# Optimization experiments

Hardware: AMD Instinct MI355X
Metric: run time of the kernel (lower is better)

Reference implementation:

```python
import jax, jax.numpy as jnp
import numpy as np

EPS = 1e-6

def rmsnorm(x, w):
    rms = jnp.sqrt(jnp.mean(x * x, axis=-1, keepdims=True) + EPS)
    return w * x / rms

def setup_inputs() -> dict:
    key = jax.random.key(0)
    k1, k2, k3 = jax.random.split(key, 3)
    S, N, B, T, D = 8, 8, 2, 2048, 1024
    return {
        "pseudo_queries": jax.random.normal(k1, (S, D), dtype=jnp.float32),
        "block_reps": jax.random.normal(k2, (N, B, T, D), dtype=jnp.float32),
        "partial_sums": jax.random.normal(k3, (S, B, T, D), dtype=jnp.float32),
        "norm_weight": jnp.ones((D,), dtype=jnp.float32),
    }

def reference(pseudo_queries, block_reps, partial_sums, norm_weight):
    D = pseudo_queries.shape[-1]
    scale = 1.0 / jnp.sqrt(jnp.asarray(D, pseudo_queries.dtype))

    # ---- Phase 1: inter-block attention over the N layers ----
    V = block_reps                               # [N,B,T,D]
    K = rmsnorm(V, norm_weight)                  # [N,B,T,D]
    logits = jnp.einsum('sd,nbtd->snbt', pseudo_queries, K) * scale  # [S,N,B,T]
    inter_max = jnp.max(logits, axis=1)          # [S,B,T]
    exp_logits = jnp.exp(logits - inter_max[:, None])
    inter_lse = jnp.log(jnp.sum(exp_logits, axis=1)) + inter_max     # [S,B,T]
    attn = jax.nn.softmax(logits, axis=1)        # [S,N,B,T]
    inter_out = jnp.einsum('snbt,nbtd->sbtd', attn, V)               # [S,B,T,D]

    # ---- Phase 2: intra-block merge (vectorized over S) ----
    K2 = rmsnorm(partial_sums, norm_weight)      # [S,B,T,D]
    intra_max = jnp.einsum('sd,sbtd->sbt', pseudo_queries, K2) * scale  # [S,B,T]
    merged_max = jnp.maximum(inter_max, intra_max)
    w_inter = jnp.exp(inter_max - merged_max)
    w_intra = jnp.exp(intra_max - merged_max)
    merged_lse = jnp.log(w_inter * jnp.exp(inter_lse - inter_max) + w_intra) + merged_max
    norm = w_inter + w_intra
    merged_out = (w_inter[..., None] * inter_out + w_intra[..., None] * partial_sums) / norm[..., None]
    return merged_out, merged_max, merged_lse
```

## Files before the change

### kernel.cpp

```cpp
#include <hip/hip_runtime.h>
#include <math.h>

#define TPB 256

template <int CTRL>
__device__ __forceinline__ float dpp_add(float x) {
    int yi = __builtin_amdgcn_update_dpp(0, __float_as_int(x), CTRL, 0xF, 0xF, true);
    return x + __int_as_float(yi);
}

__device__ __forceinline__ float wave_sum(float x) {
    x = dpp_add<0xB1>(x);
    x = dpp_add<0x4E>(x);
    x = dpp_add<0x141>(x);
    x = dpp_add<0x140>(x);
    x = dpp_add<0x142>(x);
    x = dpp_add<0x143>(x);
    return __int_as_float(__builtin_amdgcn_readlane(__float_as_int(x), 63));
}

__device__ __forceinline__ float dot4(const float4& a, const float4& b) {
    return a.x * b.x + a.y * b.y + a.z * b.z + a.w * b.w;
}

__global__ __launch_bounds__(TPB) void two_phase_attn_kernel(
    const float* __restrict__ q,
    const float* __restrict__ V,
    const float* __restrict__ P,
    const float* __restrict__ wgt,
    float* __restrict__ out)
{
    constexpr int    N   = 8;
    constexpr int    D   = 1024;
    constexpr int    BT  = 4096;
    constexpr size_t ROW = (size_t)BT * D;
    constexpr size_t OUT_MM  = (size_t)8 * ROW;
    constexpr size_t OUT_LSE = OUT_MM + (size_t)BT * 8;
    constexpr float  SCALE = 0.03125f;
    constexpr float  EPS   = 1e-6f;

    __shared__ float sV[N][D];

    const int bt   = blockIdx.x;
    const int tid  = threadIdx.x;
    const int w    = tid >> 6;
    const int lane = tid & 63;
    const int s0 = 2 * w, s1 = s0 + 1;
    const size_t btD = (size_t)bt * D;

    #pragma unroll
    for (int j = 0; j < 4; ++j) {
        const int d = j * 256 + lane * 4;
        *(float4*)(&sV[s0][d]) = *(const float4*)(V + (size_t)s0 * ROW + btD + d);
        *(float4*)(&sV[s1][d]) = *(const float4*)(V + (size_t)s1 * ROW + btD + d);
    }
    __syncthreads();

    float dot0[N], dot1[N], vsq[N];
    #pragma unroll
    for (int n = 0; n < N; ++n) { dot0[n] = 0.f; dot1[n] = 0.f; vsq[n] = 0.f; }

    #pragma unroll
    for (int j = 0; j < 4; ++j) {
        const int d = j * 256 + lane * 4;
        const float4 wv = *(const float4*)(wgt + d);
        const float4 a  = *(const float4*)(q + s0 * D + d);
        const float4 b  = *(const float4*)(q + s1 * D + d);
        const float4 qa = make_float4(a.x*wv.x, a.y*wv.y, a.z*wv.z, a.w*wv.w);
        const float4 qb = make_float4(b.x*wv.x, b.y*wv.y, b.z*wv.z, b.w*wv.w);
        #pragma unroll
        for (int n = 0; n < N; ++n) {
            const float4 v = *(const float4*)(&sV[n][d]);
            dot0[n] += dot4(qa, v);
            dot1[n] += dot4(qb, v);
            vsq[n]  += dot4(v, v);
        }
    }

    float4 p0[4], p1[4];
    #pragma unroll
    for (int j = 0; j < 4; ++j) {
        const int d = j * 256 + lane * 4;
        p0[j] = *(const float4*)(P + (size_t)s0 * ROW + btD + d);
        p1[j] = *(const float4*)(P + (size_t)s1 * ROW + btD + d);
    }

    #pragma unroll
    for (int n = 0; n < N; ++n) {
        dot0[n] = wave_sum(dot0[n]);
        dot1[n] = wave_sum(dot1[n]);
        vsq[n]  = wave_sum(vsq[n]);
    }

    float e0[N], e1[N];
    float m0 = -1e30f, m1 = -1e30f;
    #pragma unroll
    for (int n = 0; n < N; ++n) {
        const float rinv = rsqrtf(vsq[n] * (1.0f / 1024.0f) + EPS);
        e0[n] = dot0[n] * rinv * SCALE;  m0 = fmaxf(m0, e0[n]);
        e1[n] = dot1[n] * rinv * SCALE;  m1 = fmaxf(m1, e1[n]);
    }
    float es0 = 0.f, es1 = 0.f;
    #pragma unroll
    for (int n = 0; n < N; ++n) {
        e0[n] = __expf(e0[n] - m0);  es0 += e0[n];
        e1[n] = __expf(e1[n] - m1);  es1 += e1[n];
    }

    float ssq20 = 0.f, ssq21 = 0.f, dp0 = 0.f, dp1 = 0.f;
    #pragma unroll
    for (int j = 0; j < 4; ++j) {
        const int d = j * 256 + lane * 4;
        const float4 wv = *(const float4*)(wgt + d);
        const float4 a  = *(const float4*)(q + s0 * D + d);
        const float4 b  = *(const float4*)(q + s1 * D + d);
        ssq20 += dot4(p0[j], p0[j]);
        ssq21 += dot4(p1[j], p1[j]);
        dp0 += (a.x*wv.x)*p0[j].x + (a.y*wv.y)*p0[j].y + (a.z*wv.z)*p0[j].z + (a.w*wv.w)*p0[j].w;
        dp1 += (b.x*wv.x)*p1[j].x + (b.y*wv.y)*p1[j].y + (b.z*wv.z)*p1[j].z + (b.w*wv.w)*p1[j].w;
    }
    ssq20 = wave_sum(ssq20);  ssq21 = wave_sum(ssq21);
    dp0   = wave_sum(dp0);    dp1   = wave_sum(dp1);

    const float im0 = dp0 * rsqrtf(ssq20 * (1.0f/1024.0f) + EPS) * SCALE;
    const float im1 = dp1 * rsqrtf(ssq21 * (1.0f/1024.0f) + EPS) * SCALE;

    const float mm0 = fmaxf(m0, im0),    mm1 = fmaxf(m1, im1);
    const float wi0 = __expf(m0 - mm0),  wi1 = __expf(m1 - mm1);
    const float wa0 = __expf(im0 - mm0), wa1 = __expf(im1 - mm1);
    const float lse0 = __logf(wi0 * es0 + wa0) + mm0;
    const float lse1 = __logf(wi1 * es1 + wa1) + mm1;
    const float nrm0 = wi0 + wa0,        nrm1 = wi1 + wa1;
    const float cA0 = wi0 / (es0 * nrm0), cA1 = wi1 / (es1 * nrm1);
    const float cp0 = wa0 / nrm0,         cp1 = wa1 / nrm1;

    #pragma unroll
    for (int j = 0; j < 4; ++j) {
        const int d = j * 256 + lane * 4;
        float4 A0 = make_float4(0.f, 0.f, 0.f, 0.f);
        float4 A1 = make_float4(0.f, 0.f, 0.f, 0.f);
        #pragma unroll
        for (int n = 0; n < N; ++n) {
            const float4 v = *(const float4*)(&sV[n][d]);
            A0.x += e0[n]*v.x; A0.y += e0[n]*v.y; A0.z += e0[n]*v.z; A0.w += e0[n]*v.w;
            A1.x += e1[n]*v.x; A1.y += e1[n]*v.y; A1.z += e1[n]*v.z; A1.w += e1[n]*v.w;
        }
        float4 o0, o1;
        o0.x = cA0*A0.x + cp0*p0[j].x;  o0.y = cA0*A0.y + cp0*p0[j].y;
        o0.z = cA0*A0.z + cp0*p0[j].z;  o0.w = cA0*A0.w + cp0*p0[j].w;
        o1.x = cA1*A1.x + cp1*p1[j].x;  o1.y = cA1*A1.y + cp1*p1[j].y;
        o1.z = cA1*A1.z + cp1*p1[j].z;  o1.w = cA1*A1.w + cp1*p1[j].w;
        *(float4*)(out + (size_t)s0 * ROW + btD + d) = o0;
        *(float4*)(out + (size_t)s1 * ROW + btD + d) = o1;
    }
    if (lane == 0) {
        out[OUT_MM  + (size_t)s0 * BT + bt] = mm0;
        out[OUT_MM  + (size_t)s1 * BT + bt] = mm1;
        out[OUT_LSE + (size_t)s0 * BT + bt] = lse0;
        out[OUT_LSE + (size_t)s1 * BT + bt] = lse1;
    }
}

extern "C" void kernel_launch(void* const* d_in, const int* in_sizes, int n_in,
                              void* d_out, int out_size, void* d_ws, size_t ws_size,
                              hipStream_t stream) {
    const float* q   = (const float*)d_in[0];
    const float* V   = (const float*)d_in[1];
    const float* P   = (const float*)d_in[2];
    const float* wgt = (const float*)d_in[3];
    float* o = (float*)d_out;

    two_phase_attn_kernel<<<4096, TPB, 0, stream>>>(q, V, P, wgt, o);
}
```

Baseline: 105.1 us.

## Make blocks persistent over eight rows with register-prefetched V double buffering

Each block now processes eight consecutive bt rows instead of one, launching 512 blocks instead of 4096. The V row for the next iteration is prefetched into registers while the current row is computed, then written to shared memory after a barrier. This aims to hide global load latency and amortise launch and setup costs. The trade-offs are fewer resident blocks (512 blocks over the GPU's compute units), higher register pressure and an extra barrier per iteration.

```diff
diff --git a/kernel.cpp b/kernel.cpp
--- a/kernel.cpp
+++ b/kernel.cpp
@@ -1,7 +1,9 @@
 #include <hip/hip_runtime.h>
 #include <math.h>
 
-#define TPB 256
+#define TPB   256
+#define NBLK  512
+#define ITERS 8
 
 template <int CTRL>
 __device__ __forceinline__ float dpp_add(float x) {
@@ -19,8 +21,8 @@
     return __int_as_float(__builtin_amdgcn_readlane(__float_as_int(x), 63));
 }
 
-__device__ __forceinline__ float dot4(const float4& a, const float4& b) {
-    return a.x * b.x + a.y * b.y + a.z * b.z + a.w * b.w;
+__device__ __forceinline__ float dot4(const float4 a, const float4 b) {
+    return a.x*b.x + a.y*b.y + a.z*b.z + a.w*b.w;
 }
 
 __global__ __launch_bounds__(TPB) void two_phase_attn_kernel(
@@ -41,123 +43,158 @@
 
     __shared__ float sV[N][D];
 
-    const int bt   = blockIdx.x;
     const int tid  = threadIdx.x;
     const int w    = tid >> 6;
     const int lane = tid & 63;
-    const int s0 = 2 * w, s1 = s0 + 1;
-    const size_t btD = (size_t)bt * D;
-
+    const int s0 = 2*w, s1 = s0 + 1;
+    const int d0 = lane * 4;
+    const int bt0 = blockIdx.x * ITERS;
+
+    const float* Vr0 = V + (size_t)s0*ROW + (size_t)bt0*D + d0;
+    const float* Vr1 = V + (size_t)s1*ROW + (size_t)bt0*D + d0;
+    const float* Pr0 = P + (size_t)s0*ROW + (size_t)bt0*D + d0;
+    const float* Pr1 = P + (size_t)s1*ROW + (size_t)bt0*D + d0;
+    float*       Or0 = out + (size_t)s0*ROW + (size_t)bt0*D + d0;
+    float*       Or1 = out + (size_t)s1*ROW + (size_t)bt0*D + d0;
+
+    float4 vst0[4], vst1[4];
     #pragma unroll
     for (int j = 0; j < 4; ++j) {
-        const int d = j * 256 + lane * 4;
-        *(float4*)(&sV[s0][d]) = *(const float4*)(V + (size_t)s0 * ROW + btD + d);
-        *(float4*)(&sV[s1][d]) = *(const float4*)(V + (size_t)s1 * ROW + btD + d);
-    }
-    __syncthreads();
-
-    float dot0[N], dot1[N], vsq[N];
-    #pragma unroll
-    for (int n = 0; n < N; ++n) { dot0[n] = 0.f; dot1[n] = 0.f; vsq[n] = 0.f; }
-
+        vst0[j] = *(const float4*)(Vr0 + j*256);
+        vst1[j] = *(const float4*)(Vr1 + j*256);
+    }
     #pragma unroll
     for (int j = 0; j < 4; ++j) {
-        const int d = j * 256 + lane * 4;
-        const float4 wv = *(const float4*)(wgt + d);
-        const float4 a  = *(const float4*)(q + s0 * D + d);
-        const float4 b  = *(const float4*)(q + s1 * D + d);
-        const float4 qa = make_float4(a.x*wv.x, a.y*wv.y, a.z*wv.z, a.w*wv.w);
-        const float4 qb = make_float4(b.x*wv.x, b.y*wv.y, b.z*wv.z, b.w*wv.w);
-        #pragma unroll
-        for (int n = 0; n < N; ++n) {
-            const float4 v = *(const float4*)(&sV[n][d]);
-            dot0[n] += dot4(qa, v);
-            dot1[n] += dot4(qb, v);
-            vsq[n]  += dot4(v, v);
-        }
-    }
-
-    float4 p0[4], p1[4];
+        *(float4*)(&sV[s0][j*256 + d0]) = vst0[j];
+        *(float4*)(&sV[s1][j*256 + d0]) = vst1[j];
+    }
     #pragma unroll
     for (int j = 0; j < 4; ++j) {
-        const int d = j * 256 + lane * 4;
-        p0[j] = *(const float4*)(P + (size_t)s0 * ROW + btD + d);
-        p1[j] = *(const float4*)(P + (size_t)s1 * ROW + btD + d);
-    }
-
-    #pragma unroll
-    for (int n = 0; n < N; ++n) {
-        dot0[n] = wave_sum(dot0[n]);
-        dot1[n] = wave_sum(dot1[n]);
-        vsq[n]  = wave_sum(vsq[n]);
-    }
-
-    float e0[N], e1[N];
-    float m0 = -1e30f, m1 = -1e30f;
-    #pragma unroll
-    for (int n = 0; n < N; ++n) {
-        const float rinv = rsqrtf(vsq[n] * (1.0f / 1024.0f) + EPS);
-        e0[n] = dot0[n] * rinv * SCALE;  m0 = fmaxf(m0, e0[n]);
-        e1[n] = dot1[n] * rinv * SCALE;  m1 = fmaxf(m1, e1[n]);
-    }
-    float es0 = 0.f, es1 = 0.f;
-    #pragma unroll
-    for (int n = 0; n < N; ++n) {
-        e0[n] = __expf(e0[n] - m0);  es0 += e0[n];
-        e1[n] = __expf(e1[n] - m1);  es1 += e1[n];
-    }
-
-    float ssq20 = 0.f, ssq21 = 0.f, dp0 = 0.f, dp1 = 0.f;
-    #pragma unroll
-    for (int j = 0; j < 4; ++j) {
-        const int d = j * 256 + lane * 4;
-        const float4 wv = *(const float4*)(wgt + d);
-        const float4 a  = *(const float4*)(q + s0 * D + d);
-        const float4 b  = *(const float4*)(q + s1 * D + d);
-        ssq20 += dot4(p0[j], p0[j]);
-        ssq21 += dot4(p1[j], p1[j]);
-        dp0 += (a.x*wv.x)*p0[j].x + (a.y*wv.y)*p0[j].y + (a.z*wv.z)*p0[j].z + (a.w*wv.w)*p0[j].w;
-        dp1 += (b.x*wv.x)*p1[j].x + (b.y*wv.y)*p1[j].y + (b.z*wv.z)*p1[j].z + (b.w*wv.w)*p1[j].w;
-    }
-    ssq20 = wave_sum(ssq20);  ssq21 = wave_sum(ssq21);
-    dp0   = wave_sum(dp0);    dp1   = wave_sum(dp1);
-
-    const float im0 = dp0 * rsqrtf(ssq20 * (1.0f/1024.0f) + EPS) * SCALE;
-    const float im1 = dp1 * rsqrtf(ssq21 * (1.0f/1024.0f) + EPS) * SCALE;
-
-    const float mm0 = fmaxf(m0, im0),    mm1 = fmaxf(m1, im1);
-    const float wi0 = __expf(m0 - mm0),  wi1 = __expf(m1 - mm1);
-    const float wa0 = __expf(im0 - mm0), wa1 = __expf(im1 - mm1);
-    const float lse0 = __logf(wi0 * es0 + wa0) + mm0;
-    const float lse1 = __logf(wi1 * es1 + wa1) + mm1;
-    const float nrm0 = wi0 + wa0,        nrm1 = wi1 + wa1;
-    const float cA0 = wi0 / (es0 * nrm0), cA1 = wi1 / (es1 * nrm1);
-    const float cp0 = wa0 / nrm0,         cp1 = wa1 / nrm1;
-
-    #pragma unroll
-    for (int j = 0; j < 4; ++j) {
-        const int d = j * 256 + lane * 4;
-        float4 A0 = make_float4(0.f, 0.f, 0.f, 0.f);
-        float4 A1 = make_float4(0.f, 0.f, 0.f, 0.f);
+        vst0[j] = *(const float4*)(Vr0 + D + j*256);
+        vst1[j] = *(const float4*)(Vr1 + D + j*256);
+    }
+    __syncthreads();
+
+    for (int k = 0; k < ITERS; ++k) {
+        const int off = k * D;
+
+        float4 p0[4], p1[4];
+        #pragma unroll
+        for (int j = 0; j < 4; ++j) {
+            p0[j] = *(const float4*)(Pr0 + off + j*256);
+            p1[j] = *(const float4*)(Pr1 + off + j*256);
+        }
+
+        float dot0[N], dot1[N], vsq[N];
+        #pragma unroll
+        for (int n = 0; n < N; ++n) { dot0[n] = 0.f; dot1[n] = 0.f; vsq[n] = 0.f; }
+        #pragma unroll
+        for (int j = 0; j < 4; ++j) {
+            const int d = j*256 + d0;
+            const float4 wv = *(const float4*)(wgt + d);
+            const float4 a  = *(const float4*)(q + s0*D + d);
+            const float4 b  = *(const float4*)(q + s1*D + d);
+            const float4 qa = make_float4(a.x*wv.x, a.y*wv.y, a.z*wv.z, a.w*wv.w);
+            const float4 qb = make_float4(b.x*wv.x, b.y*wv.y, b.z*wv.z, b.w*wv.w);
+            #pragma unroll
+            for (int n = 0; n < N; ++n) {
+                const float4 v = *(const float4*)(&sV[n][d]);
+                dot0[n] += dot4(qa, v);
+                dot1[n] += dot4(qb, v);
+                vsq[n]  += dot4(v, v);
+            }
+        }
         #pragma unroll
         for (int n = 0; n < N; ++n) {
-            const float4 v = *(const float4*)(&sV[n][d]);
-            A0.x += e0[n]*v.x; A0.y += e0[n]*v.y; A0.z += e0[n]*v.z; A0.w += e0[n]*v.w;
-            A1.x += e1[n]*v.x; A1.y += e1[n]*v.y; A1.z += e1[n]*v.z; A1.w += e1[n]*v.w;
-        }
-        float4 o0, o1;
-        o0.x = cA0*A0.x + cp0*p0[j].x;  o0.y = cA0*A0.y + cp0*p0[j].y;
-        o0.z = cA0*A0.z + cp0*p0[j].z;  o0.w = cA0*A0.w + cp0*p0[j].w;
-        o1.x = cA1*A1.x + cp1*p1[j].x;  o1.y = cA1*A1.y + cp1*p1[j].y;
-        o1.z = cA1*A1.z + cp1*p1[j].z;  o1.w = cA1*A1.w + cp1*p1[j].w;
-        *(float4*)(out + (size_t)s0 * ROW + btD + d) = o0;
-        *(float4*)(out + (size_t)s1 * ROW + btD + d) = o1;
-    }
-    if (lane == 0) {
-        out[OUT_MM  + (size_t)s0 * BT + bt] = mm0;
-        out[OUT_MM  + (size_t)s1 * BT + bt] = mm1;
-        out[OUT_LSE + (size_t)s0 * BT + bt] = lse0;
-        out[OUT_LSE + (size_t)s1 * BT + bt] = lse1;
+            dot0[n] = wave_sum(dot0[n]);
+            dot1[n] = wave_sum(dot1[n]);
+            vsq[n]  = wave_sum(vsq[n]);
+        }
+
+        float e0[N], e1[N];
+        float m0 = -1e30f, m1 = -1e30f;
+        #pragma unroll
+        for (int n = 0; n < N; ++n) {
+            const float rinv = rsqrtf(vsq[n] * (1.0f/1024.0f) + EPS);
+            e0[n] = dot0[n] * rinv * SCALE;  m0 = fmaxf(m0, e0[n]);
+            e1[n] = dot1[n] * rinv * SCALE;  m1 = fmaxf(m1, e1[n]);
+        }
+        float es0 = 0.f, es1 = 0.f;
+        #pragma unroll
+        for (int n = 0; n < N; ++n) {
+            e0[n] = __expf(e0[n] - m0);  es0 += e0[n];
+            e1[n] = __expf(e1[n] - m1);  es1 += e1[n];
+        }
+
+        float ssq20 = 0.f, ssq21 = 0.f, dp0 = 0.f, dp1 = 0.f;
+        #pragma unroll
+        for (int j = 0; j < 4; ++j) {
+            const int d = j*256 + d0;
+            const float4 wv = *(const float4*)(wgt + d);
+            const float4 a  = *(const float4*)(q + s0*D + d);
+            const float4 b  = *(const float4*)(q + s1*D + d);
+            ssq20 += dot4(p0[j], p0[j]);
+            ssq21 += dot4(p1[j], p1[j]);
+            dp0 += (a.x*wv.x)*p0[j].x + (a.y*wv.y)*p0[j].y + (a.z*wv.z)*p0[j].z + (a.w*wv.w)*p0[j].w;
+            dp1 += (b.x*wv.x)*p1[j].x + (b.y*wv.y)*p1[j].y + (b.z*wv.z)*p1[j].z + (b.w*wv.w)*p1[j].w;
+        }
+        ssq20 = wave_sum(ssq20);  ssq21 = wave_sum(ssq21);
+        dp0   = wave_sum(dp0);    dp1   = wave_sum(dp1);
+
+        const float im0 = dp0 * rsqrtf(ssq20 * (1.0f/1024.0f) + EPS) * SCALE;
+        const float im1 = dp1 * rsqrtf(ssq21 * (1.0f/1024.0f) + EPS) * SCALE;
+        const float mm0 = fmaxf(m0, im0),    mm1 = fmaxf(m1, im1);
+        const float wi0 = __expf(m0 - mm0),  wi1 = __expf(m1 - mm1);
+        const float wa0 = __expf(im0 - mm0), wa1 = __expf(im1 - mm1);
+        const float lse0 = __logf(wi0 * es0 + wa0) + mm0;
+        const float lse1 = __logf(wi1 * es1 + wa1) + mm1;
+        const float nrm0 = wi0 + wa0,        nrm1 = wi1 + wa1;
+        const float cA0 = wi0 / (es0 * nrm0), cA1 = wi1 / (es1 * nrm1);
+        const float cp0 = wa0 / nrm0,         cp1 = wa1 / nrm1;
+
+        #pragma unroll
+        for (int j = 0; j < 4; ++j) {
+            const int d = j*256 + d0;
+            float4 A0 = make_float4(0.f,0.f,0.f,0.f);
+            float4 A1 = make_float4(0.f,0.f,0.f,0.f);
+            #pragma unroll
+            for (int n = 0; n < N; ++n) {
+                const float4 v = *(const float4*)(&sV[n][d]);
+                A0.x += e0[n]*v.x; A0.y += e0[n]*v.y; A0.z += e0[n]*v.z; A0.w += e0[n]*v.w;
+                A1.x += e1[n]*v.x; A1.y += e1[n]*v.y; A1.z += e1[n]*v.z; A1.w += e1[n]*v.w;
+            }
+            float4 o0, o1;
+            o0.x = cA0*A0.x + cp0*p0[j].x;  o0.y = cA0*A0.y + cp0*p0[j].y;
+            o0.z = cA0*A0.z + cp0*p0[j].z;  o0.w = cA0*A0.w + cp0*p0[j].w;
+            o1.x = cA1*A1.x + cp1*p1[j].x;  o1.y = cA1*A1.y + cp1*p1[j].y;
+            o1.z = cA1*A1.z + cp1*p1[j].z;  o1.w = cA1*A1.w + cp1*p1[j].w;
+            *(float4*)(Or0 + off + j*256) = o0;
+            *(float4*)(Or1 + off + j*256) = o1;
+        }
+        if (lane == 0) {
+            const int bt = bt0 + k;
+            out[OUT_MM  + (size_t)s0*BT + bt] = mm0;
+            out[OUT_MM  + (size_t)s1*BT + bt] = mm1;
+            out[OUT_LSE + (size_t)s0*BT + bt] = lse0;
+            out[OUT_LSE + (size_t)s1*BT + bt] = lse1;
+        }
+
+        __syncthreads();
+        if (k + 1 < ITERS) {
+            #pragma unroll
+            for (int j = 0; j < 4; ++j) {
+                *(float4*)(&sV[s0][j*256 + d0]) = vst0[j];
+                *(float4*)(&sV[s1][j*256 + d0]) = vst1[j];
+            }
+            if (k + 2 < ITERS) {
+                #pragma unroll
+                for (int j = 0; j < 4; ++j) {
+                    vst0[j] = *(const float4*)(Vr0 + (k+2)*D + j*256);
+                    vst1[j] = *(const float4*)(Vr1 + (k+2)*D + j*256);
+                }
+            }
+            __syncthreads();
+        }
     }
 }
 
@@ -170,5 +207,5 @@
     const float* wgt = (const float*)d_in[3];
     float* o = (float*)d_out;
 
-    two_phase_attn_kernel<<<4096, TPB, 0, stream>>>(q, V, P, wgt, o);
-}
+    two_phase_attn_kernel<<<NBLK, TPB, 0, stream>>>(q, V, P, wgt, o);
+}
```

Measured after the change: 164.9 us. +56.9%, slower.

## Use one wave per pseudo-query and compute V sum-of-squares once per row

Applied to the files above, without the earlier changes.

The block grows from 4 to 8 waves, so each wave handles a single pseudo-query instead of two. Each wave loads its own V and P rows into registers and computes the V squared norm once, sharing it through shared memory. This removes the redundant per-wave recomputation of all eight V norms and halves per-thread register state, which should allow more waves in flight to hide memory latency. The cost is more waves contending for LDS reads and a larger block per bt, and the launch_bounds hint of 8 may constrain register allocation.

```diff
diff --git a/kernel.cpp b/kernel.cpp
--- a/kernel.cpp
+++ b/kernel.cpp
@@ -1,7 +1,7 @@
 #include <hip/hip_runtime.h>
 #include <math.h>
 
-#define TPB 256
+#define TPB 512
 
 template <int CTRL>
 __device__ __forceinline__ float dpp_add(float x) {
@@ -19,11 +19,11 @@
     return __int_as_float(__builtin_amdgcn_readlane(__float_as_int(x), 63));
 }
 
-__device__ __forceinline__ float dot4(const float4& a, const float4& b) {
-    return a.x * b.x + a.y * b.y + a.z * b.z + a.w * b.w;
+__device__ __forceinline__ float dot4(const float4 a, const float4 b) {
+    return a.x*b.x + a.y*b.y + a.z*b.z + a.w*b.w;
 }
 
-__global__ __launch_bounds__(TPB) void two_phase_attn_kernel(
+__global__ __launch_bounds__(TPB, 8) void two_phase_attn_kernel(
     const float* __restrict__ q,
     const float* __restrict__ V,
     const float* __restrict__ P,
@@ -40,124 +40,103 @@
     constexpr float  EPS   = 1e-6f;
 
     __shared__ float sV[N][D];
+    __shared__ float sSsq[N];
 
-    const int bt   = blockIdx.x;
     const int tid  = threadIdx.x;
     const int w    = tid >> 6;
     const int lane = tid & 63;
-    const int s0 = 2 * w, s1 = s0 + 1;
+    const int d0   = lane * 4;
+    const int bt   = blockIdx.x;
     const size_t btD = (size_t)bt * D;
+
+    const float* Vr = V   + (size_t)w * ROW + btD + d0;
+    const float* Pr = P   + (size_t)w * ROW + btD + d0;
+    float*       Or = out + (size_t)w * ROW + btD + d0;
+
+    float4 v[4], p[4], qw[4];
+    #pragma unroll
+    for (int j = 0; j < 4; ++j) v[j] = *(const float4*)(Vr + j*256);
+    #pragma unroll
+    for (int j = 0; j < 4; ++j) p[j] = *(const float4*)(Pr + j*256);
+    #pragma unroll
+    for (int j = 0; j < 4; ++j) {
+        const int d = j*256 + d0;
+        const float4 a  = *(const float4*)(q + w*D + d);
+        const float4 wv = *(const float4*)(wgt + d);
+        qw[j] = make_float4(a.x*wv.x, a.y*wv.y, a.z*wv.z, a.w*wv.w);
+    }
+
+    float vsq = 0.f;
+    #pragma unroll
+    for (int j = 0; j < 4; ++j) {
+        *(float4*)(&sV[w][j*256 + d0]) = v[j];
+        vsq += dot4(v[j], v[j]);
+    }
+    vsq = wave_sum(vsq);
+    if (lane == 0) sSsq[w] = vsq;
+    __syncthreads();
+
+    float dt[N];
+    #pragma unroll
+    for (int n = 0; n < N; ++n) dt[n] = 0.f;
+    #pragma unroll
+    for (int j = 0; j < 4; ++j) {
+        const int d = j*256 + d0;
+        #pragma unroll
+        for (int n = 0; n < N; ++n)
+            dt[n] += dot4(qw[j], *(const float4*)(&sV[n][d]));
+    }
+    #pragma unroll
+    for (int n = 0; n < N; ++n) dt[n] = wave_sum(dt[n]);
+
+    float m = -1e30f;
+    #pragma unroll
+    for (int n = 0; n < N; ++n) {
+        const float rinv = rsqrtf(sSsq[n] * (1.0f/1024.0f) + EPS);
+        dt[n] = dt[n] * rinv * SCALE;
+        m = fmaxf(m, dt[n]);
+    }
+    float es = 0.f;
+    #pragma unroll
+    for (int n = 0; n < N; ++n) { dt[n] = __expf(dt[n] - m); es += dt[n]; }
+
+    float ssq2 = 0.f, dp = 0.f;
+    #pragma unroll
+    for (int j = 0; j < 4; ++j) {
+        ssq2 += dot4(p[j], p[j]);
+        dp   += dot4(qw[j], p[j]);
+    }
+    ssq2 = wave_sum(ssq2);
+    dp   = wave_sum(dp);
+
+    const float im  = dp * rsqrtf(ssq2 * (1.0f/1024.0f) + EPS) * SCALE;
+    const float mm  = fmaxf(m, im);
+    const float wi  = __expf(m  - mm);
+    const float wa  = __expf(im - mm);
+    const float lse = __logf(wi * es + wa) + mm;
+    const float nrm = wi + wa;
+    const float cA  = wi / (es * nrm);
+    const float cp  = wa / nrm;
 
     #pragma unroll
     for (int j = 0; j < 4; ++j) {
-        const int d = j * 256 + lane * 4;
-        *(float4*)(&sV[s0][d]) = *(const float4*)(V + (size_t)s0 * ROW + btD + d);
-        *(float4*)(&sV[s1][d]) = *(const float4*)(V + (size_t)s1 * ROW + btD + d);
-    }
-    __syncthreads();
-
-    float dot0[N], dot1[N], vsq[N];
-    #pragma unroll
-    for (int n = 0; n < N; ++n) { dot0[n] = 0.f; dot1[n] = 0.f; vsq[n] = 0.f; }
-
-    #pragma unroll
-    for (int j = 0; j < 4; ++j) {
-        const int d = j * 256 + lane * 4;
-        const float4 wv = *(const float4*)(wgt + d);
-        const float4 a  = *(const float4*)(q + s0 * D + d);
-        const float4 b  = *(const float4*)(q + s1 * D + d);
-        const float4 qa = make_float4(a.x*wv.x, a.y*wv.y, a.z*wv.z, a.w*wv.w);
-        const float4 qb = make_float4(b.x*wv.x, b.y*wv.y, b.z*wv.z, b.w*wv.w);
+        const int d = j*256 + d0;
+        float4 A = make_float4(0.f, 0.f, 0.f, 0.f);
         #pragma unroll
         for (int n = 0; n < N; ++n) {
-            const float4 v = *(const float4*)(&sV[n][d]);
-            dot0[n] += dot4(qa, v);
-            dot1[n] += dot4(qb, v);
-            vsq[n]  += dot4(v, v);
+            const float4 vv = *(const float4*)(&sV[n][d]);
+            A.x += dt[n]*vv.x; A.y += dt[n]*vv.y; A.z += dt[n]*vv.z; A.w += dt[n]*vv.w;
         }
-    }
-
-    float4 p0[4], p1[4];
-    #pragma unroll
-    for (int j = 0; j < 4; ++j) {
-        const int d = j * 256 + lane * 4;
-        p0[j] = *(const float4*)(P + (size_t)s0 * ROW + btD + d);
-        p1[j] = *(const float4*)(P + (size_t)s1 * ROW + btD + d);
-    }
-
-    #pragma unroll
-    for (int n = 0; n < N; ++n) {
-        dot0[n] = wave_sum(dot0[n]);
-        dot1[n] = wave_sum(dot1[n]);
-        vsq[n]  = wave_sum(vsq[n]);
-    }
-
-    float e0[N], e1[N];
-    float m0 = -1e30f, m1 = -1e30f;
-    #pragma unroll
-    for (int n = 0; n < N; ++n) {
-        const float rinv = rsqrtf(vsq[n] * (1.0f / 1024.0f) + EPS);
-        e0[n] = dot0[n] * rinv * SCALE;  m0 = fmaxf(m0, e0[n]);
-        e1[n] = dot1[n] * rinv * SCALE;  m1 = fmaxf(m1, e1[n]);
-    }
-    float es0 = 0.f, es1 = 0.f;
-    #pragma unroll
-    for (int n = 0; n < N; ++n) {
-        e0[n] = __expf(e0[n] - m0);  es0 += e0[n];
-        e1[n] = __expf(e1[n] - m1);  es1 += e1[n];
-    }
-
-    float ssq20 = 0.f, ssq21 = 0.f, dp0 = 0.f, dp1 = 0.f;
-    #pragma unroll
-    for (int j = 0; j < 4; ++j) {
-        const int d = j * 256 + lane * 4;
-        const float4 wv = *(const float4*)(wgt + d);
-        const float4 a  = *(const float4*)(q + s0 * D + d);
-        const float4 b  = *(const float4*)(q + s1 * D + d);
-        ssq20 += dot4(p0[j], p0[j]);
-        ssq21 += dot4(p1[j], p1[j]);
-        dp0 += (a.x*wv.x)*p0[j].x + (a.y*wv.y)*p0[j].y + (a.z*wv.z)*p0[j].z + (a.w*wv.w)*p0[j].w;
-        dp1 += (b.x*wv.x)*p1[j].x + (b.y*wv.y)*p1[j].y + (b.z*wv.z)*p1[j].z + (b.w*wv.w)*p1[j].w;
-    }
-    ssq20 = wave_sum(ssq20);  ssq21 = wave_sum(ssq21);
-    dp0   = wave_sum(dp0);    dp1   = wave_sum(dp1);
-
-    const float im0 = dp0 * rsqrtf(ssq20 * (1.0f/1024.0f) + EPS) * SCALE;
-    const float im1 = dp1 * rsqrtf(ssq21 * (1.0f/1024.0f) + EPS) * SCALE;
-
-    const float mm0 = fmaxf(m0, im0),    mm1 = fmaxf(m1, im1);
-    const float wi0 = __expf(m0 - mm0),  wi1 = __expf(m1 - mm1);
-    const float wa0 = __expf(im0 - mm0), wa1 = __expf(im1 - mm1);
-    const float lse0 = __logf(wi0 * es0 + wa0) + mm0;
-    const float lse1 = __logf(wi1 * es1 + wa1) + mm1;
-    const float nrm0 = wi0 + wa0,        nrm1 = wi1 + wa1;
-    const float cA0 = wi0 / (es0 * nrm0), cA1 = wi1 / (es1 * nrm1);
-    const float cp0 = wa0 / nrm0,         cp1 = wa1 / nrm1;
-
-    #pragma unroll
-    for (int j = 0; j < 4; ++j) {
-        const int d = j * 256 + lane * 4;
-        float4 A0 = make_float4(0.f, 0.f, 0.f, 0.f);
-        float4 A1 = make_float4(0.f, 0.f, 0.f, 0.f);
-        #pragma unroll
-        for (int n = 0; n < N; ++n) {
-            const float4 v = *(const float4*)(&sV[n][d]);
-            A0.x += e0[n]*v.x; A0.y += e0[n]*v.y; A0.z += e0[n]*v.z; A0.w += e0[n]*v.w;
-            A1.x += e1[n]*v.x; A1.y += e1[n]*v.y; A1.z += e1[n]*v.z; A1.w += e1[n]*v.w;
-        }
-        float4 o0, o1;
-        o0.x = cA0*A0.x + cp0*p0[j].x;  o0.y = cA0*A0.y + cp0*p0[j].y;
-        o0.z = cA0*A0.z + cp0*p0[j].z;  o0.w = cA0*A0.w + cp0*p0[j].w;
-        o1.x = cA1*A1.x + cp1*p1[j].x;  o1.y = cA1*A1.y + cp1*p1[j].y;
-        o1.z = cA1*A1.z + cp1*p1[j].z;  o1.w = cA1*A1.w + cp1*p1[j].w;
-        *(float4*)(out + (size_t)s0 * ROW + btD + d) = o0;
-        *(float4*)(out + (size_t)s1 * ROW + btD + d) = o1;
+        float4 o;
+        o.x = cA*A.x + cp*p[j].x;
+        o.y = cA*A.y + cp*p[j].y;
+        o.z = cA*A.z + cp*p[j].z;
+        o.w = cA*A.w + cp*p[j].w;
+        *(float4*)(Or + j*256) = o;
     }
     if (lane == 0) {
-        out[OUT_MM  + (size_t)s0 * BT + bt] = mm0;
-        out[OUT_MM  + (size_t)s1 * BT + bt] = mm1;
-        out[OUT_LSE + (size_t)s0 * BT + bt] = lse0;
-        out[OUT_LSE + (size_t)s1 * BT + bt] = lse1;
+        out[OUT_MM  + (size_t)w * BT + bt] = mm;
+        out[OUT_LSE + (size_t)w * BT + bt] = lse;
     }
 }
 
```

Measured after the change: 147.3 us. 1.4x slower.

## Split work per (bt, s-pair) block with V held in registers

Applied to the files above, without the earlier changes.

Launches four blocks per token, each handling one pair of pseudo-queries across the full hidden dimension with one float4 per thread, instead of one block per token staging all layer rows in shared memory. V rows are kept in registers and partial dot products are reduced across waves through a small shared buffer. This removes the large shared-memory footprint to raise occupancy, and adds a launch bound hint. The cost is that each token's V rows are read by four blocks, relying on cache to absorb the extra traffic, plus a block-wide reduction and barrier.

```diff
diff --git a/kernel.cpp b/kernel.cpp
--- a/kernel.cpp
+++ b/kernel.cpp
@@ -19,11 +19,11 @@
     return __int_as_float(__builtin_amdgcn_readlane(__float_as_int(x), 63));
 }
 
-__device__ __forceinline__ float dot4(const float4& a, const float4& b) {
-    return a.x * b.x + a.y * b.y + a.z * b.z + a.w * b.w;
+__device__ __forceinline__ float dot4(const float4 a, const float4 b) {
+    return a.x*b.x + a.y*b.y + a.z*b.z + a.w*b.w;
 }
 
-__global__ __launch_bounds__(TPB) void two_phase_attn_kernel(
+__global__ __launch_bounds__(TPB, 4) void two_phase_attn_kernel(
     const float* __restrict__ q,
     const float* __restrict__ V,
     const float* __restrict__ P,
@@ -31,74 +31,70 @@
     float* __restrict__ out)
 {
     constexpr int    N   = 8;
+    constexpr int    BT  = 4096;
     constexpr int    D   = 1024;
-    constexpr int    BT  = 4096;
     constexpr size_t ROW = (size_t)BT * D;
     constexpr size_t OUT_MM  = (size_t)8 * ROW;
     constexpr size_t OUT_LSE = OUT_MM + (size_t)BT * 8;
     constexpr float  SCALE = 0.03125f;
     constexpr float  EPS   = 1e-6f;
 
-    __shared__ float sV[N][D];
+    __shared__ float red[28][4];
 
-    const int bt   = blockIdx.x;
     const int tid  = threadIdx.x;
     const int w    = tid >> 6;
     const int lane = tid & 63;
-    const int s0 = 2 * w, s1 = s0 + 1;
+    const int idx  = blockIdx.x;
+    const int bt   = idx >> 2;
+    const int sp   = idx & 3;
+    const int s0   = 2*sp, s1 = 2*sp + 1;
+    const int d0   = tid * 4;
     const size_t btD = (size_t)bt * D;
 
+    float4 v[N];
     #pragma unroll
-    for (int j = 0; j < 4; ++j) {
-        const int d = j * 256 + lane * 4;
-        *(float4*)(&sV[s0][d]) = *(const float4*)(V + (size_t)s0 * ROW + btD + d);
-        *(float4*)(&sV[s1][d]) = *(const float4*)(V + (size_t)s1 * ROW + btD + d);
+    for (int n = 0; n < N; ++n)
+        v[n] = *(const float4*)(V + (size_t)n * ROW + btD + d0);
+    const float4 p0 = *(const float4*)(P + (size_t)s0 * ROW + btD + d0);
+    const float4 p1 = *(const float4*)(P + (size_t)s1 * ROW + btD + d0);
+    const float4 a0 = *(const float4*)(q + s0 * D + d0);
+    const float4 a1 = *(const float4*)(q + s1 * D + d0);
+    const float4 wv = *(const float4*)(wgt + d0);
+    const float4 qw0 = make_float4(a0.x*wv.x, a0.y*wv.y, a0.z*wv.z, a0.w*wv.w);
+    const float4 qw1 = make_float4(a1.x*wv.x, a1.y*wv.y, a1.z*wv.z, a1.w*wv.w);
+
+    float r[28];
+    #pragma unroll
+    for (int n = 0; n < N; ++n) {
+        r[n]      = dot4(qw0, v[n]);
+        r[8 + n]  = dot4(qw1, v[n]);
+        r[16 + n] = dot4(v[n], v[n]);
+    }
+    r[24] = dot4(p0, p0);
+    r[25] = dot4(p1, p1);
+    r[26] = dot4(qw0, p0);
+    r[27] = dot4(qw1, p1);
+
+    #pragma unroll
+    for (int i = 0; i < 28; ++i) r[i] = wave_sum(r[i]);
+    if (lane == 0) {
+        #pragma unroll
+        for (int i = 0; i < 28; ++i) red[i][w] = r[i];
     }
     __syncthreads();
-
-    float dot0[N], dot1[N], vsq[N];
     #pragma unroll
-    for (int n = 0; n < N; ++n) { dot0[n] = 0.f; dot1[n] = 0.f; vsq[n] = 0.f; }
-
-    #pragma unroll
-    for (int j = 0; j < 4; ++j) {
-        const int d = j * 256 + lane * 4;
-        const float4 wv = *(const float4*)(wgt + d);
-        const float4 a  = *(const float4*)(q + s0 * D + d);
-        const float4 b  = *(const float4*)(q + s1 * D + d);
-        const float4 qa = make_float4(a.x*wv.x, a.y*wv.y, a.z*wv.z, a.w*wv.w);
-        const float4 qb = make_float4(b.x*wv.x, b.y*wv.y, b.z*wv.z, b.w*wv.w);
-        #pragma unroll
-        for (int n = 0; n < N; ++n) {
-            const float4 v = *(const float4*)(&sV[n][d]);
-            dot0[n] += dot4(qa, v);
-            dot1[n] += dot4(qb, v);
-            vsq[n]  += dot4(v, v);
-        }
-    }
-
-    float4 p0[4], p1[4];
-    #pragma unroll
-    for (int j = 0; j < 4; ++j) {
-        const int d = j * 256 + lane * 4;
-        p0[j] = *(const float4*)(P + (size_t)s0 * ROW + btD + d);
-        p1[j] = *(const float4*)(P + (size_t)s1 * ROW + btD + d);
-    }
-
-    #pragma unroll
-    for (int n = 0; n < N; ++n) {
-        dot0[n] = wave_sum(dot0[n]);
-        dot1[n] = wave_sum(dot1[n]);
-        vsq[n]  = wave_sum(vsq[n]);
+    for (int i = 0; i < 28; ++i) {
+        const float4 t = *(const float4*)(&red[i][0]);
+        r[i] = t.x + t.y + t.z + t.w;
     }
 
     float e0[N], e1[N];
     float m0 = -1e30f, m1 = -1e30f;
     #pragma unroll
     for (int n = 0; n < N; ++n) {
-        const float rinv = rsqrtf(vsq[n] * (1.0f / 1024.0f) + EPS);
-        e0[n] = dot0[n] * rinv * SCALE;  m0 = fmaxf(m0, e0[n]);
-        e1[n] = dot1[n] * rinv * SCALE;  m1 = fmaxf(m1, e1[n]);
+        const float rinv = rsqrtf(r[16 + n] * (1.0f/1024.0f) + EPS);
+        e0[n] = r[n]     * rinv * SCALE;  m0 = fmaxf(m0, e0[n]);
+        e1[n] = r[8 + n] * rinv * SCALE;  m1 = fmaxf(m1, e1[n]);
     }
     float es0 = 0.f, es1 = 0.f;
     #pragma unroll
@@ -107,53 +103,33 @@
         e1[n] = __expf(e1[n] - m1);  es1 += e1[n];
     }
 
-    float ssq20 = 0.f, ssq21 = 0.f, dp0 = 0.f, dp1 = 0.f;
-    #pragma unroll
-    for (int j = 0; j < 4; ++j) {
-        const int d = j * 256 + lane * 4;
-        const float4 wv = *(const float4*)(wgt + d);
-        const float4 a  = *(const float4*)(q + s0 * D + d);
-        const float4 b  = *(const float4*)(q + s1 * D + d);
-        ssq20 += dot4(p0[j], p0[j]);
-        ssq21 += dot4(p1[j], p1[j]);
-        dp0 += (a.x*wv.x)*p0[j].x + (a.y*wv.y)*p0[j].y + (a.z*wv.z)*p0[j].z + (a.w*wv.w)*p0[j].w;
-        dp1 += (b.x*wv.x)*p1[j].x + (b.y*wv.y)*p1[j].y + (b.z*wv.z)*p1[j].z + (b.w*wv.w)*p1[j].w;
-    }
-    ssq20 = wave_sum(ssq20);  ssq21 = wave_sum(ssq21);
-    dp0   = wave_sum(dp0);    dp1   = wave_sum(dp1);
-
-    const float im0 = dp0 * rsqrtf(ssq20 * (1.0f/1024.0f) + EPS) * SCALE;
-    const float im1 = dp1 * rsqrtf(ssq21 * (1.0f/1024.0f) + EPS) * SCALE;
-
+    const float im0 = r[26] * rsqrtf(r[24] * (1.0f/1024.0f) + EPS) * SCALE;
+    const float im1 = r[27] * rsqrtf(r[25] * (1.0f/1024.0f) + EPS) * SCALE;
     const float mm0 = fmaxf(m0, im0),    mm1 = fmaxf(m1, im1);
     const float wi0 = __expf(m0 - mm0),  wi1 = __expf(m1 - mm1);
     const float wa0 = __expf(im0 - mm0), wa1 = __expf(im1 - mm1);
     const float lse0 = __logf(wi0 * es0 + wa0) + mm0;
     const float lse1 = __logf(wi1 * es1 + wa1) + mm1;
-    const float nrm0 = wi0 + wa0,        nrm1 = wi1 + wa1;
+    const float nrm0 = wi0 + wa0,         nrm1 = wi1 + wa1;
     const float cA0 = wi0 / (es0 * nrm0), cA1 = wi1 / (es1 * nrm1);
     const float cp0 = wa0 / nrm0,         cp1 = wa1 / nrm1;
 
+    float4 A0 = make_float4(0.f,0.f,0.f,0.f);
+    float4 A1 = make_float4(0.f,0.f,0.f,0.f);
     #pragma unroll
-    for (int j = 0; j < 4; ++j) {
-        const int d = j * 256 + lane * 4;
-        float4 A0 = make_float4(0.f, 0.f, 0.f, 0.f);
-        float4 A1 = make_float4(0.f, 0.f, 0.f, 0.f);
-        #pragma unroll
-        for (int n = 0; n < N; ++n) {
-            const float4 v = *(const float4*)(&sV[n][d]);
-            A0.x += e0[n]*v.x; A0.y += e0[n]*v.y; A0.z += e0[n]*v.z; A0.w += e0[n]*v.w;
-            A1.x += e1[n]*v.x; A1.y += e1[n]*v.y; A1.z += e1[n]*v.z; A1.w += e1[n]*v.w;
-        }
-        float4 o0, o1;
-        o0.x = cA0*A0.x + cp0*p0[j].x;  o0.y = cA0*A0.y + cp0*p0[j].y;
-        o0.z = cA0*A0.z + cp0*p0[j].z;  o0.w = cA0*A0.w + cp0*p0[j].w;
-        o1.x = cA1*A1.x + cp1*p1[j].x;  o1.y = cA1*A1.y + cp1*p1[j].y;
-        o1.z = cA1*A1.z + cp1*p1[j].z;  o1.w = cA1*A1.w + cp1*p1[j].w;
-        *(float4*)(out + (size_t)s0 * ROW + btD + d) = o0;
-        *(float4*)(out + (size_t)s1 * ROW + btD + d) = o1;
+    for (int n = 0; n < N; ++n) {
+        A0.x += e0[n]*v[n].x; A0.y += e0[n]*v[n].y; A0.z += e0[n]*v[n].z; A0.w += e0[n]*v[n].w;
+        A1.x += e1[n]*v[n].x; A1.y += e1[n]*v[n].y; A1.z += e1[n]*v[n].z; A1.w += e1[n]*v[n].w;
     }
-    if (lane == 0) {
+    float4 o0, o1;
+    o0.x = cA0*A0.x + cp0*p0.x;  o0.y = cA0*A0.y + cp0*p0.y;
+    o0.z = cA0*A0.z + cp0*p0.z;  o0.w = cA0*A0.w + cp0*p0.w;
+    o1.x = cA1*A1.x + cp1*p1.x;  o1.y = cA1*A1.y + cp1*p1.y;
+    o1.z = cA1*A1.z + cp1*p1.z;  o1.w = cA1*A1.w + cp1*p1.w;
+    *(float4*)(out + (size_t)s0 * ROW + btD + d0) = o0;
+    *(float4*)(out + (size_t)s1 * ROW + btD + d0) = o1;
+
+    if (tid == 0) {
         out[OUT_MM  + (size_t)s0 * BT + bt] = mm0;
         out[OUT_MM  + (size_t)s1 * BT + bt] = mm1;
         out[OUT_LSE + (size_t)s0 * BT + bt] = lse0;
@@ -170,5 +146,5 @@
     const float* wgt = (const float*)d_in[3];
     float* o = (float*)d_out;
 
-    two_phase_attn_kernel<<<4096, TPB, 0, stream>>>(q, V, P, wgt, o);
+    two_phase_attn_kernel<<<4096 * 4, TPB, 0, stream>>>(q, V, P, wgt, o);
 }
```

After: 141.1 us. 34.3% more time.
